# Optimization experiments

Measured on AMD Instinct MI355X. Metric: run time of the kernel, lower is better.

The kernel has to match this reference:

```python
import jax, jax.numpy as jnp
import numpy as np

D = 128       # in_features
H = 256       # hidden
OUT = 128     # out_features
NUM_STEPS = 3
K = 8         # k_neighbors (k = min(K, N))


def setup_inputs() -> dict:
    key = jax.random.key(0)
    ks = jax.random.split(key, 12)
    s = 0.02
    return {
        "x":    jax.random.normal(ks[0], (4, 4096, D), dtype=jnp.float32),
        # neighbor_proj: Linear(D -> H)
        "Wn":   jax.random.normal(ks[1], (D, H), dtype=jnp.float32) * s,
        "bn":   jnp.zeros((H,), dtype=jnp.float32),
        # local_rule[0]: Linear(D + H -> H)
        "W1":   jax.random.normal(ks[2], (D + H, H), dtype=jnp.float32) * s,
        "b1":   jnp.zeros((H,), dtype=jnp.float32),
        # local_rule[1]: LayerNorm(H)
        "ln_g": jnp.ones((H,), dtype=jnp.float32),
        "ln_b": jnp.zeros((H,), dtype=jnp.float32),
        # local_rule[3]: Linear(H -> D)
        "W2":   jax.random.normal(ks[3], (H, D), dtype=jnp.float32) * s,
        "b2":   jnp.zeros((D,), dtype=jnp.float32),
        # out_proj: Linear(D -> OUT)
        "Wo":   jax.random.normal(ks[4], (D, OUT), dtype=jnp.float32) * s,
        "bo":   jnp.zeros((OUT,), dtype=jnp.float32),
    }


def _layernorm(h, g, b, eps=1e-5):
    mu = jnp.mean(h, axis=-1, keepdims=True)
    var = jnp.var(h, axis=-1, keepdims=True)
    return (h - mu) * jax.lax.rsqrt(var + eps) * g + b


def reference(x, Wn, bn, W1, b1, ln_g, ln_b, W2, b2, Wo, bo):
    B, N, _ = x.shape
    k = min(K, N)
    batch_ix = jnp.arange(B)[:, None, None]  # (B,1,1)
    state = x
    for _ in range(NUM_STEPS):
        keys = state @ Wn + bn                                     # (B,N,H)
        keys = keys / jnp.maximum(
            jnp.linalg.norm(keys, axis=-1, keepdims=True), 1e-12)  # F.normalize
        sim = jnp.einsum('bnh,bmh->bnm', keys, keys)               # (B,N,N)
        _, idx = jax.lax.top_k(sim, k)                             # (B,N,k)
        gathered = state[batch_ix, idx]                            # (B,N,k,D)
        neighbor_agg = gathered.mean(axis=2) @ Wn + bn             # (B,N,H)
        combined = jnp.concatenate([state, neighbor_agg], axis=-1) # (B,N,D+H)
        h = _layernorm(combined @ W1 + b1, ln_g, ln_b)
        update = jax.nn.silu(h) @ W2 + b2                          # (B,N,D)
        state = state + update
    return state.mean(axis=1) @ Wo + bo                            # (B,OUT)
```

## Files before the change

kernel.cpp:

```cpp
#include <hip/hip_runtime.h>

#define DDIM 128
#define HDIM 256
#define BQ   4
#define NN   4096
#define RTOT (BQ*NN)

typedef short short8 __attribute__((ext_vector_type(8)));
typedef short short4v __attribute__((ext_vector_type(4)));
typedef float f32x16 __attribute__((ext_vector_type(16)));

__device__ inline unsigned short f2bf(float f) {
    unsigned int u = __float_as_uint(f);
    unsigned int r = (u + 0x7fffu + ((u >> 16) & 1u)) >> 16;
    return (unsigned short)r;
}
__device__ inline float bf2f(unsigned short h) {
    return __uint_as_float(((unsigned int)h) << 16);
}

#define MFMA32(a, b, c) __builtin_amdgcn_mfma_f32_32x32x16_bf16(a, b, c, 0, 0, 0)

__global__ void pack_w_kernel(const float* __restrict__ W, int N,
                              unsigned short* __restrict__ ph, unsigned short* __restrict__ pl) {
    int l = threadIdx.x, l31 = l & 31, lh = l >> 5;
    int nt = N >> 5;
    int t = blockIdx.x / nt, c = blockIdx.x % nt;
    short8 hv, lv;
#pragma unroll
    for (int j = 0; j < 8; ++j) {
        float f = W[(size_t)(t * 16 + lh * 8 + j) * N + c * 32 + l31];
        unsigned short h = f2bf(f);
        hv[j] = (short)h;
        lv[j] = (short)f2bf(f - bf2f(h));
    }
    *(short8*)(ph + (size_t)(blockIdx.x * 64 + l) * 8) = hv;
    *(short8*)(pl + (size_t)(blockIdx.x * 64 + l) * 8) = lv;
}

__global__ __launch_bounds__(256, 2)
void sim_topk_kernel(const unsigned short* __restrict__ khi,
                     const unsigned short* __restrict__ klo,
                     int* __restrict__ idxout) {
    __shared__ __align__(16) char smem[4 * 3 * 4096];

    const int id = blockIdx.x;
    const int xcd = id & 7;
    const int b = xcd >> 1;
    const int j = ((id >> 3) << 1) | (xcd & 1);
    const int rowbase = j * 32;
    const unsigned short* khiB = khi + (size_t)b * NN * HDIM;
    const unsigned short* kloB = klo + (size_t)b * NN * HDIM;

    const int tid = threadIdx.x;
    const int lane = tid & 63, w = tid >> 6;
    const int l31 = lane & 31, lh = lane >> 5;

    short8 ah[16], al[16];
    {
        const unsigned short* ph = khiB + (size_t)(rowbase + l31) * HDIM + lh * 8;
        const unsigned short* pl = kloB + (size_t)(rowbase + l31) * HDIM + lh * 8;
#pragma unroll
        for (int T = 0; T < 16; ++T) {
            ah[T] = *(const short8*)(ph + T * 16);
            al[T] = *(const short8*)(pl + T * 16);
        }
    }
#pragma unroll
    for (int T = 0; T < 16; ++T) {
        asm volatile("" : "+v"(ah[T]));
        asm volatile("" : "+v"(al[T]));
    }

    char* mybuf = smem + w * 12288;

    const int sc = lane >> 2, sg = lane & 3;
    const int ssw = (sg ^ ((sc >> 1) & 3)) * 8;
    auto stage = [&](int s) {
        const int cs2 = s >> 3, ks2 = s & 7;
        char* dst = mybuf + (s % 3) * 4096;
        const int c0 = w * 1024 + cs2 * 32;
#pragma unroll
        for (int p = 0; p < 2; ++p) {
            const unsigned short* pb = p ? kloB : khiB;
#pragma unroll
            for (int i = 0; i < 2; ++i) {
                const unsigned short* src = pb + (size_t)(c0 + i * 16 + sc) * HDIM + ks2 * 32 + ssw;
                __builtin_amdgcn_global_load_lds(
                    (const __attribute__((address_space(1))) void*)src,
                    (__attribute__((address_space(3))) void*)(dst + p * 2048 + i * 1024), 16, 0, 0);
            }
        }
    };

    stage(0);
    stage(1);

    const int key = (l31 >> 1) & 3;
    const int rb0 = l31 * 64 + ((lh ^ key) * 16);
    const int rb1 = l31 * 64 + (((2 + lh) ^ key) * 16);

    float tv[8]; int ti[8];
#pragma unroll
    for (int s = 0; s < 8; ++s) { tv[s] = -1e30f; ti[s] = 0x7fffffff; }

    for (int cs = 0; cs < 32; ++cs) {
        f32x16 acc;
#pragma unroll
        for (int r = 0; r < 16; ++r) acc[r] = 0.f;

#pragma unroll
        for (int ks = 0; ks < 8; ++ks) {
            const int s = cs * 8 + ks;
            if (s < 255) asm volatile("s_waitcnt vmcnt(4)" ::: "memory");
            else         asm volatile("s_waitcnt vmcnt(0)" ::: "memory");

            const char* bufc = mybuf + (s % 3) * 4096;
            short8 Bh0 = *(const short8*)(bufc + rb0);
            short8 Bl0 = *(const short8*)(bufc + 2048 + rb0);
            short8 Bh1 = *(const short8*)(bufc + rb1);
            short8 Bl1 = *(const short8*)(bufc + 2048 + rb1);
            asm volatile("s_waitcnt lgkmcnt(4)" ::: "memory");
            if (s + 2 < 256) stage(s + 2);

            const int T0 = ks * 2, T1 = ks * 2 + 1;
            acc = MFMA32(Bh0, ah[T0], acc);
            acc = MFMA32(Bh0, al[T0], acc);
            acc = MFMA32(Bl0, ah[T0], acc);
            acc = MFMA32(Bh1, ah[T1], acc);
            acc = MFMA32(Bh1, al[T1], acc);
            acc = MFMA32(Bl1, ah[T1], acc);
        }

        const int cbase = w * 1024 + cs * 32 + 4 * lh;
#pragma unroll
        for (int r = 0; r < 16; ++r) {
            float v = acc[r];
            int col = cbase + (r & 3) + 8 * (r >> 2);
            if (v > tv[7]) {
                tv[7] = v; ti[7] = col;
#pragma unroll
                for (int q = 7; q >= 1; --q) {
                    if (tv[q] > tv[q - 1]) {
                        float a0 = tv[q]; tv[q] = tv[q - 1]; tv[q - 1] = a0;
                        int   c0_ = ti[q]; ti[q] = ti[q - 1]; ti[q - 1] = c0_;
                    }
                }
            }
        }
    }

    __syncthreads();
    float* vbuf = (float*)smem;
    int*   ibuf = (int*)(smem + 32 * 66 * 4);
    const int list = w * 2 + lh;
#pragma unroll
    for (int s = 0; s < 8; ++s) {
        vbuf[l31 * 66 + list * 8 + s] = tv[s];
        ibuf[l31 * 66 + list * 8 + s] = ti[s];
    }
    __syncthreads();
    if (tid < 32) {
        float fv[8]; int fi[8];
#pragma unroll
        for (int s = 0; s < 8; ++s) { fv[s] = -1e30f; fi[s] = 0x7fffffff; }
        for (int e = 0; e < 64; ++e) {
            float v = vbuf[tid * 66 + e];
            int  ix = ibuf[tid * 66 + e];
            bool ins = (v > fv[7]) || (v == fv[7] && ix < fi[7]);
            if (ins) {
                fv[7] = v; fi[7] = ix;
#pragma unroll
                for (int q = 7; q >= 1; --q) {
                    bool sw = (fv[q] > fv[q - 1]) || (fv[q] == fv[q - 1] && fi[q] < fi[q - 1]);
                    if (sw) {
                        float a0 = fv[q]; fv[q] = fv[q - 1]; fv[q - 1] = a0;
                        int   c0_ = fi[q]; fi[q] = fi[q - 1]; fi[q - 1] = c0_;
                    }
                }
            }
        }
        size_t basei = ((size_t)b * NN + rowbase + tid) * 8;
#pragma unroll
        for (int s = 0; s < 8; ++s) idxout[basei + s] = fi[s];
    }
}

__global__ __launch_bounds__(256, 2)
void gemm_keys_mfma(const float* __restrict__ A,
                    const unsigned short* __restrict__ wh, const unsigned short* __restrict__ wl,
                    const float* __restrict__ bias,
                    unsigned short* __restrict__ khi, unsigned short* __restrict__ klo) {
    __shared__ float ssqbuf[2][32][2];
    const int tid = threadIdx.x, lane = tid & 63, w = tid >> 6;
    const int l31 = lane & 31, lh = lane >> 5;
    const int rw = w & 1, cw = w >> 1;
    const int row = blockIdx.x * 64 + rw * 32 + l31;

    short8 ahi[8], alo[8];
    const float* ap = A + (size_t)row * DDIM + lh * 8;
#pragma unroll
    for (int T = 0; T < 8; ++T) {
        float4 f0 = *(const float4*)(ap + T * 16);
        float4 f1 = *(const float4*)(ap + T * 16 + 4);
        float ff[8] = {f0.x, f0.y, f0.z, f0.w, f1.x, f1.y, f1.z, f1.w};
#pragma unroll
        for (int j2 = 0; j2 < 8; ++j2) {
            unsigned short h = f2bf(ff[j2]);
            ahi[T][j2] = (short)h;
            alo[T][j2] = (short)f2bf(ff[j2] - bf2f(h));
        }
    }

    f32x16 acc[4];
#pragma unroll
    for (int ct = 0; ct < 4; ++ct)
#pragma unroll
        for (int r = 0; r < 16; ++r) acc[ct][r] = 0.f;

#pragma unroll
    for (int T = 0; T < 8; ++T) {
#pragma unroll
        for (int ct = 0; ct < 4; ++ct) {
            const size_t pi = (size_t)((T * 8 + cw * 4 + ct) * 64 + lane) * 8;
            short8 bh = *(const short8*)(wh + pi);
            short8 bl = *(const short8*)(wl + pi);
            acc[ct] = MFMA32(bh, ahi[T], acc[ct]);
            acc[ct] = MFMA32(bl, ahi[T], acc[ct]);
            acc[ct] = MFMA32(bh, alo[T], acc[ct]);
        }
    }

    float ss = 0.f;
#pragma unroll
    for (int ct = 0; ct < 4; ++ct)
#pragma unroll
        for (int g = 0; g < 4; ++g) {
            const int c0 = cw * 128 + ct * 32 + g * 8 + lh * 4;
            float4 bz = *(const float4*)(bias + c0);
            float bzf[4] = {bz.x, bz.y, bz.z, bz.w};
#pragma unroll
            for (int j2 = 0; j2 < 4; ++j2) {
                acc[ct][g * 4 + j2] += bzf[j2];
                ss += acc[ct][g * 4 + j2] * acc[ct][g * 4 + j2];
            }
        }
    ss += __shfl_xor(ss, 32);
    if (lh == 0) ssqbuf[rw][l31][cw] = ss;
    __syncthreads();
    float sstot = ssqbuf[rw][l31][0] + ssqbuf[rw][l31][1];
    float scn = 1.0f / fmaxf(sqrtf(sstot), 1e-12f);

#pragma unroll
    for (int ct = 0; ct < 4; ++ct)
#pragma unroll
        for (int g = 0; g < 4; ++g) {
            const int c0 = cw * 128 + ct * 32 + g * 8 + lh * 4;
            short4v hv, lv;
#pragma unroll
            for (int j2 = 0; j2 < 4; ++j2) {
                float vn = acc[ct][g * 4 + j2] * scn;
                unsigned short h = f2bf(vn);
                hv[j2] = (short)h;
                lv[j2] = (short)f2bf(vn - bf2f(h));
            }
            *(short4v*)(khi + (size_t)row * HDIM + c0) = hv;
            *(short4v*)(klo + (size_t)row * HDIM + c0) = lv;
        }
}

__global__ __launch_bounds__(256, 2)
void gemm_agg_mfma(const float* __restrict__ A,
                   const unsigned short* __restrict__ wh, const unsigned short* __restrict__ wl,
                   const float* __restrict__ bias,
                   unsigned short* __restrict__ oh, unsigned short* __restrict__ ol) {
    const int tid = threadIdx.x, lane = tid & 63, w = tid >> 6;
    const int l31 = lane & 31, lh = lane >> 5;
    const int rw = w & 1, cw = w >> 1;
    const int row = blockIdx.x * 64 + rw * 32 + l31;

    short8 ahi[8], alo[8];
    const float* ap = A + (size_t)row * DDIM + lh * 8;
#pragma unroll
    for (int T = 0; T < 8; ++T) {
        float4 f0 = *(const float4*)(ap + T * 16);
        float4 f1 = *(const float4*)(ap + T * 16 + 4);
        float ff[8] = {f0.x, f0.y, f0.z, f0.w, f1.x, f1.y, f1.z, f1.w};
#pragma unroll
        for (int j2 = 0; j2 < 8; ++j2) {
            unsigned short h = f2bf(ff[j2]);
            ahi[T][j2] = (short)h;
            alo[T][j2] = (short)f2bf(ff[j2] - bf2f(h));
        }
    }

    f32x16 acc[4];
#pragma unroll
    for (int ct = 0; ct < 4; ++ct)
#pragma unroll
        for (int r = 0; r < 16; ++r) acc[ct][r] = 0.f;

#pragma unroll
    for (int T = 0; T < 8; ++T) {
#pragma unroll
        for (int ct = 0; ct < 4; ++ct) {
            const size_t pi = (size_t)((T * 8 + cw * 4 + ct) * 64 + lane) * 8;
            short8 bh = *(const short8*)(wh + pi);
            short8 bl = *(const short8*)(wl + pi);
            acc[ct] = MFMA32(bh, ahi[T], acc[ct]);
            acc[ct] = MFMA32(bl, ahi[T], acc[ct]);
            acc[ct] = MFMA32(bh, alo[T], acc[ct]);
        }
    }

#pragma unroll
    for (int ct = 0; ct < 4; ++ct)
#pragma unroll
        for (int g = 0; g < 4; ++g) {
            const int c0 = cw * 128 + ct * 32 + g * 8 + lh * 4;
            float4 bz = *(const float4*)(bias + c0);
            float bzf[4] = {bz.x, bz.y, bz.z, bz.w};
            short4v hv, lv;
#pragma unroll
            for (int j2 = 0; j2 < 4; ++j2) {
                float vn = acc[ct][g * 4 + j2] + bzf[j2];
                unsigned short h = f2bf(vn);
                hv[j2] = (short)h;
                lv[j2] = (short)f2bf(vn - bf2f(h));
            }
            *(short4v*)(oh + (size_t)row * HDIM + c0) = hv;
            *(short4v*)(ol + (size_t)row * HDIM + c0) = lv;
        }
}

__global__ __launch_bounds__(256, 2)
void gemm_ln_mfma(const float* __restrict__ state,
                  const unsigned short* __restrict__ agh, const unsigned short* __restrict__ agl,
                  const unsigned short* __restrict__ wh, const unsigned short* __restrict__ wl,
                  const float* __restrict__ b1, const float* __restrict__ lng,
                  const float* __restrict__ lnb,
                  unsigned short* __restrict__ gh, unsigned short* __restrict__ gl) {
    __shared__ float s1buf[2][32][2], s2buf[2][32][2];
    const int tid = threadIdx.x, lane = tid & 63, w = tid >> 6;
    const int l31 = lane & 31, lh = lane >> 5;
    const int rw = w & 1, cw = w >> 1;
    const int row = blockIdx.x * 64 + rw * 32 + l31;

    f32x16 acc[4];
#pragma unroll
    for (int ct = 0; ct < 4; ++ct)
#pragma unroll
        for (int r = 0; r < 16; ++r) acc[ct][r] = 0.f;

    short8 ahi[8], alo[8];
    {
        const float* ap = state + (size_t)row * DDIM + lh * 8;
#pragma unroll
        for (int T = 0; T < 8; ++T) {
            float4 f0 = *(const float4*)(ap + T * 16);
            float4 f1 = *(const float4*)(ap + T * 16 + 4);
            float ff[8] = {f0.x, f0.y, f0.z, f0.w, f1.x, f1.y, f1.z, f1.w};
#pragma unroll
            for (int j2 = 0; j2 < 8; ++j2) {
                unsigned short h = f2bf(ff[j2]);
                ahi[T][j2] = (short)h;
                alo[T][j2] = (short)f2bf(ff[j2] - bf2f(h));
            }
        }
#pragma unroll
        for (int T = 0; T < 8; ++T)
#pragma unroll
            for (int ct = 0; ct < 4; ++ct) {
                const size_t pi = (size_t)((T * 8 + cw * 4 + ct) * 64 + lane) * 8;
                short8 bh = *(const short8*)(wh + pi);
                short8 bl = *(const short8*)(wl + pi);
                acc[ct] = MFMA32(bh, ahi[T], acc[ct]);
                acc[ct] = MFMA32(bl, ahi[T], acc[ct]);
                acc[ct] = MFMA32(bh, alo[T], acc[ct]);
            }
    }
#pragma unroll
    for (int kc = 1; kc < 3; ++kc) {
#pragma unroll
        for (int T = 0; T < 8; ++T) {
            ahi[T] = *(const short8*)(agh + (size_t)row * HDIM + (kc - 1) * 128 + T * 16 + lh * 8);
            alo[T] = *(const short8*)(agl + (size_t)row * HDIM + (kc - 1) * 128 + T * 16 + lh * 8);
        }
#pragma unroll
        for (int T = 0; T < 8; ++T)
#pragma unroll
            for (int ct = 0; ct < 4; ++ct) {
                const size_t pi = (size_t)(((kc * 8 + T) * 8 + cw * 4 + ct) * 64 + lane) * 8;
                short8 bh = *(const short8*)(wh + pi);
                short8 bl = *(const short8*)(wl + pi);
                acc[ct] = MFMA32(bh, ahi[T], acc[ct]);
                acc[ct] = MFMA32(bl, ahi[T], acc[ct]);
                acc[ct] = MFMA32(bh, alo[T], acc[ct]);
            }
    }

    float s1 = 0.f, s2 = 0.f;
#pragma unroll
    for (int ct = 0; ct < 4; ++ct)
#pragma unroll
        for (int g = 0; g < 4; ++g) {
            const int c0 = cw * 128 + ct * 32 + g * 8 + lh * 4;
            float4 bz = *(const float4*)(b1 + c0);
            float bzf[4] = {bz.x, bz.y, bz.z, bz.w};
#pragma unroll
            for (int j2 = 0; j2 < 4; ++j2) {
                acc[ct][g * 4 + j2] += bzf[j2];
                s1 += acc[ct][g * 4 + j2];
                s2 += acc[ct][g * 4 + j2] * acc[ct][g * 4 + j2];
            }
        }
    s1 += __shfl_xor(s1, 32);
    s2 += __shfl_xor(s2, 32);
    if (lh == 0) { s1buf[rw][l31][cw] = s1; s2buf[rw][l31][cw] = s2; }
    __syncthreads();
    float s1t = s1buf[rw][l31][0] + s1buf[rw][l31][1];
    float s2t = s2buf[rw][l31][0] + s2buf[rw][l31][1];
    float mu = s1t * (1.0f / HDIM);
    float var = s2t * (1.0f / HDIM) - mu * mu;
    float inv = 1.0f / sqrtf(var + 1e-5f);

#pragma unroll
    for (int ct = 0; ct < 4; ++ct)
#pragma unroll
        for (int g = 0; g < 4; ++g) {
            const int c0 = cw * 128 + ct * 32 + g * 8 + lh * 4;
            float4 gg = *(const float4*)(lng + c0);
            float4 bb = *(const float4*)(lnb + c0);
            float ggf[4] = {gg.x, gg.y, gg.z, gg.w};
            float bbf[4] = {bb.x, bb.y, bb.z, bb.w};
            short4v hv, lv;
#pragma unroll
            for (int j2 = 0; j2 < 4; ++j2) {
                float hval = (acc[ct][g * 4 + j2] - mu) * inv * ggf[j2] + bbf[j2];
                float gval = hval / (1.0f + expf(-hval));
                unsigned short h = f2bf(gval);
                hv[j2] = (short)h;
                lv[j2] = (short)f2bf(gval - bf2f(h));
            }
            *(short4v*)(gh + (size_t)row * HDIM + c0) = hv;
            *(short4v*)(gl + (size_t)row * HDIM + c0) = lv;
        }
}

__global__ __launch_bounds__(256, 2)
void gemm_upd_mfma(const unsigned short* __restrict__ gh, const unsigned short* __restrict__ gl,
                   const unsigned short* __restrict__ wh, const unsigned short* __restrict__ wl,
                   const float* __restrict__ b2, float* __restrict__ state) {
    const int tid = threadIdx.x, lane = tid & 63, w = tid >> 6;
    const int l31 = lane & 31, lh = lane >> 5;
    const int rw = w & 1, cw = w >> 1;
    const int row = blockIdx.x * 64 + rw * 32 + l31;

    f32x16 acc[2];
#pragma unroll
    for (int ct = 0; ct < 2; ++ct)
#pragma unroll
        for (int r = 0; r < 16; ++r) acc[ct][r] = 0.f;

    short8 ahi[8], alo[8];
#pragma unroll
    for (int kc = 0; kc < 2; ++kc) {
#pragma unroll
        for (int T = 0; T < 8; ++T) {
            ahi[T] = *(const short8*)(gh + (size_t)row * HDIM + kc * 128 + T * 16 + lh * 8);
            alo[T] = *(const short8*)(gl + (size_t)row * HDIM + kc * 128 + T * 16 + lh * 8);
        }
#pragma unroll
        for (int T = 0; T < 8; ++T)
#pragma unroll
            for (int ct = 0; ct < 2; ++ct) {
                const size_t pi = (size_t)(((kc * 8 + T) * 4 + cw * 2 + ct) * 64 + lane) * 8;
                short8 bh = *(const short8*)(wh + pi);
                short8 bl = *(const short8*)(wl + pi);
                acc[ct] = MFMA32(bh, ahi[T], acc[ct]);
                acc[ct] = MFMA32(bl, ahi[T], acc[ct]);
                acc[ct] = MFMA32(bh, alo[T], acc[ct]);
            }
    }

#pragma unroll
    for (int ct = 0; ct < 2; ++ct)
#pragma unroll
        for (int g = 0; g < 4; ++g) {
            const int c0 = cw * 64 + ct * 32 + g * 8 + lh * 4;
            float4 bz = *(const float4*)(b2 + c0);
            float bzf[4] = {bz.x, bz.y, bz.z, bz.w};
            float4* sp = (float4*)(state + (size_t)row * DDIM + c0);
            float4 sv = *sp;
            float svf[4] = {sv.x, sv.y, sv.z, sv.w};
#pragma unroll
            for (int j2 = 0; j2 < 4; ++j2) svf[j2] += acc[ct][g * 4 + j2] + bzf[j2];
            sv.x = svf[0]; sv.y = svf[1]; sv.z = svf[2]; sv.w = svf[3];
            *sp = sv;
        }
}

__global__ void gather_mean_kernel(const float* __restrict__ state, const int* __restrict__ idx,
                                   float* __restrict__ M) {
    __shared__ int ilds[16];
    int tid = threadIdx.x;
    int row0 = blockIdx.x * 2;
    if (tid < 16) ilds[tid] = idx[(size_t)row0 * 8 + tid];
    __syncthreads();
    int lr = tid >> 7, d = tid & 127;
    int grow = row0 + lr;
    int b = grow >> 12;
    const float* sb = state + (size_t)b * NN * DDIM;
    float acc = 0.f;
#pragma unroll
    for (int k = 0; k < 8; ++k) acc += sb[(size_t)ilds[lr * 8 + k] * DDIM + d];
    M[(size_t)grow * DDIM + d] = acc * 0.125f;
}

__global__ void partial_mean_kernel(const float* __restrict__ state, float* __restrict__ partial) {
    int b = blockIdx.y, seg = blockIdx.x, tid = threadIdx.x;
    const float* sp = state + ((size_t)b * NN + (size_t)seg * 128) * DDIM;
    float acc = 0.f;
    for (int i = 0; i < 128; ++i) acc += sp[(size_t)i * DDIM + tid];
    partial[((size_t)b * 32 + seg) * DDIM + tid] = acc;
}

__global__ void final_out_kernel(const float* __restrict__ partial, const float* __restrict__ Wo,
                                 const float* __restrict__ bo, float* __restrict__ out) {
    __shared__ float mean[BQ][DDIM];
    int tid = threadIdx.x;
    for (int o = tid; o < BQ * DDIM; o += 256) {
        int b = o >> 7, d = o & 127;
        float s = 0.f;
        for (int p = 0; p < 32; ++p) s += partial[((size_t)b * 32 + p) * DDIM + d];
        mean[b][d] = s * (1.0f / NN);
    }
    __syncthreads();
    for (int o = tid; o < BQ * DDIM; o += 256) {
        int b = o >> 7, c = o & 127;
        float acc = bo[c];
        for (int d = 0; d < DDIM; ++d) acc += mean[b][d] * Wo[d * DDIM + c];
        out[o] = acc;
    }
}

extern "C" void kernel_launch(void* const* d_in, const int* in_sizes, int n_in,
                              void* d_out, int out_size, void* d_ws, size_t ws_size,
                              hipStream_t stream) {
    const float* x   = (const float*)d_in[0];
    const float* Wn  = (const float*)d_in[1];
    const float* bn  = (const float*)d_in[2];
    const float* W1  = (const float*)d_in[3];
    const float* b1  = (const float*)d_in[4];
    const float* lng = (const float*)d_in[5];
    const float* lnb = (const float*)d_in[6];
    const float* W2  = (const float*)d_in[7];
    const float* b2  = (const float*)d_in[8];
    const float* Wo  = (const float*)d_in[9];
    const float* bo  = (const float*)d_in[10];
    float* out = (float*)d_out;

    float* ws    = (float*)d_ws;
    float* state = ws;
    unsigned short* agghi = (unsigned short*)(state + (size_t)RTOT * DDIM);
    unsigned short* agglo = agghi + (size_t)RTOT * HDIM;
    unsigned short* khi_b = agglo + (size_t)RTOT * HDIM;
    unsigned short* klo_b = khi_b + (size_t)RTOT * HDIM;
    float* Mbuf = (float*)khi_b;
    unsigned short* ghi = khi_b;
    unsigned short* glo = klo_b;
    float* partial = (float*)(klo_b + (size_t)RTOT * HDIM);
    int*   idxbuf  = (int*)(partial + (size_t)BQ * 32 * DDIM);
    unsigned short* wnh = (unsigned short*)(idxbuf + (size_t)RTOT * 8);
    unsigned short* wnl = wnh + 128 * 256;
    unsigned short* w1h = wnl + 128 * 256;
    unsigned short* w1l = w1h + 384 * 256;
    unsigned short* w2h = w1l + 384 * 256;
    unsigned short* w2l = w2h + 256 * 128;

    hipMemcpyAsync(state, x, (size_t)RTOT * DDIM * sizeof(float),
                   hipMemcpyDeviceToDevice, stream);

    pack_w_kernel<<<(128 / 16) * (256 / 32), 64, 0, stream>>>(Wn, 256, wnh, wnl);
    pack_w_kernel<<<(384 / 16) * (256 / 32), 64, 0, stream>>>(W1, 256, w1h, w1l);
    pack_w_kernel<<<(256 / 16) * (128 / 32), 64, 0, stream>>>(W2, 128, w2h, w2l);

    for (int step = 0; step < 3; ++step) {
        gemm_keys_mfma<<<RTOT / 64, 256, 0, stream>>>(state, wnh, wnl, bn, khi_b, klo_b);
        sim_topk_kernel<<<512, 256, 0, stream>>>(khi_b, klo_b, idxbuf);
        gather_mean_kernel<<<RTOT / 2, 256, 0, stream>>>(state, idxbuf, Mbuf);
        gemm_agg_mfma<<<RTOT / 64, 256, 0, stream>>>(Mbuf, wnh, wnl, bn, agghi, agglo);
        gemm_ln_mfma<<<RTOT / 64, 256, 0, stream>>>(state, agghi, agglo, w1h, w1l,
                                                    b1, lng, lnb, ghi, glo);
        gemm_upd_mfma<<<RTOT / 64, 256, 0, stream>>>(ghi, glo, w2h, w2l, b2, state);
    }
    partial_mean_kernel<<<dim3(32, BQ), 128, 0, stream>>>(state, partial);
    final_out_kernel<<<1, 256, 0, stream>>>(partial, Wo, bo, out);
}
```

Before: 857.8 us.

## Split sim/top-k over column halves and fuse top-k merge and gather into agg GEMM

The similarity/top-k kernel now splits each 32-row group's 4096 key columns across two blocks (1024 blocks instead of 512), each writing a partial top-8 of values and indices. The aggregation GEMM merges the two partial lists by rank counting, gathers the 8 neighbor state rows itself and averages them, which removes the separate gather_mean kernel and its intermediate buffer. This doubles parallelism in the dominant sim kernel to fill more CUs, at the cost of partial-result traffic, redundant per-thread gathers inside the GEMM, and extra register pressure there.

```diff
diff --git a/kernel.cpp b/kernel.cpp
--- a/kernel.cpp
+++ b/kernel.cpp
@@ -41,14 +41,17 @@
 __global__ __launch_bounds__(256, 2)
 void sim_topk_kernel(const unsigned short* __restrict__ khi,
                      const unsigned short* __restrict__ klo,
-                     int* __restrict__ idxout) {
+                     float* __restrict__ svals, int* __restrict__ sidx) {
     __shared__ __align__(16) char smem[4 * 3 * 4096];
 
     const int id = blockIdx.x;
     const int xcd = id & 7;
     const int b = xcd >> 1;
     const int j = ((id >> 3) << 1) | (xcd & 1);
-    const int rowbase = j * 32;
+    const int rowgroup = j >> 1;
+    const int ch = j & 1;
+    const int rowbase = rowgroup * 32;
+    const int colbase = ch * 2048;
     const unsigned short* khiB = khi + (size_t)b * NN * HDIM;
     const unsigned short* kloB = klo + (size_t)b * NN * HDIM;
 
@@ -79,7 +82,7 @@
     auto stage = [&](int s) {
         const int cs2 = s >> 3, ks2 = s & 7;
         char* dst = mybuf + (s % 3) * 4096;
-        const int c0 = w * 1024 + cs2 * 32;
+        const int c0 = colbase + w * 512 + cs2 * 32;
 #pragma unroll
         for (int p = 0; p < 2; ++p) {
             const unsigned short* pb = p ? kloB : khiB;
@@ -104,7 +107,7 @@
 #pragma unroll
     for (int s = 0; s < 8; ++s) { tv[s] = -1e30f; ti[s] = 0x7fffffff; }
 
-    for (int cs = 0; cs < 32; ++cs) {
+    for (int cs = 0; cs < 16; ++cs) {
         f32x16 acc;
 #pragma unroll
         for (int r = 0; r < 16; ++r) acc[r] = 0.f;
@@ -112,7 +115,7 @@
 #pragma unroll
         for (int ks = 0; ks < 8; ++ks) {
             const int s = cs * 8 + ks;
-            if (s < 255) asm volatile("s_waitcnt vmcnt(4)" ::: "memory");
+            if (s < 127) asm volatile("s_waitcnt vmcnt(4)" ::: "memory");
             else         asm volatile("s_waitcnt vmcnt(0)" ::: "memory");
 
             const char* bufc = mybuf + (s % 3) * 4096;
@@ -121,7 +124,7 @@
             short8 Bh1 = *(const short8*)(bufc + rb1);
             short8 Bl1 = *(const short8*)(bufc + 2048 + rb1);
             asm volatile("s_waitcnt lgkmcnt(4)" ::: "memory");
-            if (s + 2 < 256) stage(s + 2);
+            if (s + 2 < 128) stage(s + 2);
 
             const int T0 = ks * 2, T1 = ks * 2 + 1;
             acc = MFMA32(Bh0, ah[T0], acc);
@@ -132,7 +135,7 @@
             acc = MFMA32(Bl1, ah[T1], acc);
         }
 
-        const int cbase = w * 1024 + cs * 32 + 4 * lh;
+        const int cbase = colbase + w * 512 + cs * 32 + 4 * lh;
 #pragma unroll
         for (int r = 0; r < 16; ++r) {
             float v = acc[r];
@@ -180,9 +183,9 @@
                 }
             }
         }
-        size_t basei = ((size_t)b * NN + rowbase + tid) * 8;
-#pragma unroll
-        for (int s = 0; s < 8; ++s) idxout[basei + s] = fi[s];
+        const size_t lb = ((size_t)(b * NN + rowbase + tid) * 2 + ch) * 8;
+#pragma unroll
+        for (int s = 0; s < 8; ++s) { svals[lb + s] = fv[s]; sidx[lb + s] = fi[s]; }
     }
 }
 
@@ -270,27 +273,67 @@
 }
 
 __global__ __launch_bounds__(256, 2)
-void gemm_agg_mfma(const float* __restrict__ A,
+void gemm_agg_mfma(const float* __restrict__ state,
+                   const float* __restrict__ svals, const int* __restrict__ sidx,
                    const unsigned short* __restrict__ wh, const unsigned short* __restrict__ wl,
                    const float* __restrict__ bias,
                    unsigned short* __restrict__ oh, unsigned short* __restrict__ ol) {
+    __shared__ int mslot[256][8];
     const int tid = threadIdx.x, lane = tid & 63, w = tid >> 6;
     const int l31 = lane & 31, lh = lane >> 5;
     const int rw = w & 1, cw = w >> 1;
     const int row = blockIdx.x * 64 + rw * 32 + l31;
+    const int bb = row >> 12;
+    const float* sb = state + (size_t)bb * NN * DDIM;
+
+    int ridx[8];
+    {
+        const size_t lb = (size_t)row * 16;
+        float av[8], bv[8]; int ai[8], bi2[8];
+#pragma unroll
+        for (int k = 0; k < 8; ++k) {
+            av[k] = svals[lb + k];     ai[k]  = sidx[lb + k];
+            bv[k] = svals[lb + 8 + k]; bi2[k] = sidx[lb + 8 + k];
+        }
+        int* ms = mslot[tid];
+#pragma unroll
+        for (int i2 = 0; i2 < 8; ++i2) {
+            int r = i2;
+#pragma unroll
+            for (int j2 = 0; j2 < 8; ++j2)
+                r += ((bv[j2] > av[i2]) || (bv[j2] == av[i2] && bi2[j2] < ai[i2])) ? 1 : 0;
+            if (r < 8) ms[r] = ai[i2];
+        }
+#pragma unroll
+        for (int j2 = 0; j2 < 8; ++j2) {
+            int r = j2;
+#pragma unroll
+            for (int i2 = 0; i2 < 8; ++i2)
+                r += ((av[i2] > bv[j2]) || (av[i2] == bv[j2] && ai[i2] < bi2[j2])) ? 1 : 0;
+            if (r < 8) ms[r] = bi2[j2];
+        }
+#pragma unroll
+        for (int k = 0; k < 8; ++k) ridx[k] = ms[k];
+    }
 
     short8 ahi[8], alo[8];
-    const float* ap = A + (size_t)row * DDIM + lh * 8;
 #pragma unroll
     for (int T = 0; T < 8; ++T) {
-        float4 f0 = *(const float4*)(ap + T * 16);
-        float4 f1 = *(const float4*)(ap + T * 16 + 4);
-        float ff[8] = {f0.x, f0.y, f0.z, f0.w, f1.x, f1.y, f1.z, f1.w};
+        float fr[8] = {0.f, 0.f, 0.f, 0.f, 0.f, 0.f, 0.f, 0.f};
+#pragma unroll
+        for (int k = 0; k < 8; ++k) {
+            const float* rp = sb + (size_t)ridx[k] * DDIM + T * 16 + lh * 8;
+            float4 f0 = *(const float4*)rp;
+            float4 f1 = *(const float4*)(rp + 4);
+            fr[0] += f0.x; fr[1] += f0.y; fr[2] += f0.z; fr[3] += f0.w;
+            fr[4] += f1.x; fr[5] += f1.y; fr[6] += f1.z; fr[7] += f1.w;
+        }
 #pragma unroll
         for (int j2 = 0; j2 < 8; ++j2) {
-            unsigned short h = f2bf(ff[j2]);
+            float v = fr[j2] * 0.125f;
+            unsigned short h = f2bf(v);
             ahi[T][j2] = (short)h;
-            alo[T][j2] = (short)f2bf(ff[j2] - bf2f(h));
+            alo[T][j2] = (short)f2bf(v - bf2f(h));
         }
     }
 
@@ -498,23 +541,6 @@
             sv.x = svf[0]; sv.y = svf[1]; sv.z = svf[2]; sv.w = svf[3];
             *sp = sv;
         }
-}
-
-__global__ void gather_mean_kernel(const float* __restrict__ state, const int* __restrict__ idx,
-                                   float* __restrict__ M) {
-    __shared__ int ilds[16];
-    int tid = threadIdx.x;
-    int row0 = blockIdx.x * 2;
-    if (tid < 16) ilds[tid] = idx[(size_t)row0 * 8 + tid];
-    __syncthreads();
-    int lr = tid >> 7, d = tid & 127;
-    int grow = row0 + lr;
-    int b = grow >> 12;
-    const float* sb = state + (size_t)b * NN * DDIM;
-    float acc = 0.f;
-#pragma unroll
-    for (int k = 0; k < 8; ++k) acc += sb[(size_t)ilds[lr * 8 + k] * DDIM + d];
-    M[(size_t)grow * DDIM + d] = acc * 0.125f;
 }
 
 __global__ void partial_mean_kernel(const float* __restrict__ state, float* __restrict__ partial) {
@@ -566,12 +592,12 @@
     unsigned short* agglo = agghi + (size_t)RTOT * HDIM;
     unsigned short* khi_b = agglo + (size_t)RTOT * HDIM;
     unsigned short* klo_b = khi_b + (size_t)RTOT * HDIM;
-    float* Mbuf = (float*)khi_b;
     unsigned short* ghi = khi_b;
     unsigned short* glo = klo_b;
     float* partial = (float*)(klo_b + (size_t)RTOT * HDIM);
-    int*   idxbuf  = (int*)(partial + (size_t)BQ * 32 * DDIM);
-    unsigned short* wnh = (unsigned short*)(idxbuf + (size_t)RTOT * 8);
+    float* svals   = partial + (size_t)BQ * 32 * DDIM;
+    int*   sidx    = (int*)(svals + (size_t)RTOT * 16);
+    unsigned short* wnh = (unsigned short*)(sidx + (size_t)RTOT * 16);
     unsigned short* wnl = wnh + 128 * 256;
     unsigned short* w1h = wnl + 128 * 256;
     unsigned short* w1l = w1h + 384 * 256;
@@ -587,9 +613,9 @@
 
     for (int step = 0; step < 3; ++step) {
         gemm_keys_mfma<<<RTOT / 64, 256, 0, stream>>>(state, wnh, wnl, bn, khi_b, klo_b);
-        sim_topk_kernel<<<512, 256, 0, stream>>>(khi_b, klo_b, idxbuf);
-        gather_mean_kernel<<<RTOT / 2, 256, 0, stream>>>(state, idxbuf, Mbuf);
-        gemm_agg_mfma<<<RTOT / 64, 256, 0, stream>>>(Mbuf, wnh, wnl, bn, agghi, agglo);
+        sim_topk_kernel<<<1024, 256, 0, stream>>>(khi_b, klo_b, svals, sidx);
+        gemm_agg_mfma<<<RTOT / 64, 256, 0, stream>>>(state, svals, sidx, wnh, wnl, bn,
+                                                     agghi, agglo);
         gemm_ln_mfma<<<RTOT / 64, 256, 0, stream>>>(state, agghi, agglo, w1h, w1l,
                                                     b1, lng, lnb, ghi, glo);
         gemm_upd_mfma<<<RTOT / 64, 256, 0, stream>>>(ghi, glo, w2h, w2l, b2, state);
```

Result: slower. 1.035 ms (+20.6%).
